# Kernel tuning notes

Measured on AMD Instinct MI355X. Metric: run time of the kernel, lower is better.

## Reference

```python
import jax, jax.numpy as jnp
import numpy as np

B, N, C = 4, 2048, 1024
H = 16
D = C // H  # 64
SCALE = D ** -0.5


def setup_inputs() -> dict:
    key = jax.random.key(0)
    ks = jax.random.split(key, 5)
    x = jax.random.normal(ks[0], (B, N, C), dtype=jnp.float32)
    qkv_w = jax.random.normal(ks[1], (3 * C, C), dtype=jnp.float32) * (C ** -0.5)
    qkv_b = jax.random.normal(ks[2], (3 * C,), dtype=jnp.float32) * 0.02
    bias_mask = jnp.zeros((3 * C,), dtype=jnp.float32)  # registered buffer, zeros
    proj_w = jax.random.normal(ks[3], (C, C), dtype=jnp.float32) * (C ** -0.5)
    proj_b = jax.random.normal(ks[4], (C,), dtype=jnp.float32) * 0.02
    return {"x": x, "qkv_w": qkv_w, "qkv_b": qkv_b, "bias_mask": bias_mask,
            "proj_w": proj_w, "proj_b": proj_b}


def reference(x, qkv_w, qkv_b, bias_mask, proj_w, proj_b):
    b, n, c = x.shape
    # qkv linear with masked bias (bias_mask is zeros -> effective zero bias)
    bias = qkv_b * bias_mask
    qkv = jnp.einsum('bnc,oc->bno', x, qkv_w) + bias  # [b, n, 3c]
    qkv = qkv.reshape(b, n, 3, H, D).transpose(2, 0, 3, 1, 4)  # [3, b, h, n, d]
    q, k, v = qkv[0], qkv[1], qkv[2]
    # explicit softmax attention (rope=None path)
    attn = jnp.einsum('bhqd,bhkd->bhqk', q, k) * SCALE  # [b, h, n, n]
    attn = jax.nn.softmax(attn, axis=-1)
    out = jnp.einsum('bhqk,bhkd->bhqd', attn, v)  # [b, h, n, d]
    out = out.transpose(0, 2, 1, 3).reshape(b, n, c)
    return jnp.einsum('bnc,oc->bno', out, proj_w) + proj_b
```

## Files before the change

kernel.cpp:

```cpp
#include <hip/hip_runtime.h>
#include <hip/hip_bf16.h>

#define B_ 4
#define N_ 2048
#define C_ 1024
#define H_ 16
#define D_ 64
#define QSCALE_ 0.1803368801f

typedef _Float16 f16;
typedef __attribute__((ext_vector_type(8))) _Float16 f16x8;
typedef __attribute__((ext_vector_type(4))) _Float16 f16x4;
typedef __attribute__((ext_vector_type(4))) float f32x4;
typedef __attribute__((ext_vector_type(16))) float f32x16;
typedef __attribute__((ext_vector_type(4))) int i32x4;
#define MFMA16(a, b, c) __builtin_amdgcn_mfma_f32_16x16x32_f16(a, b, c, 0, 0, 0)
#define MFMA32(a, b, c) __builtin_amdgcn_mfma_f32_32x32x16_f16(a, b, c, 0, 0, 0)

__device__ inline void gload_lds16(const f16* g, f16* l) {
    __builtin_amdgcn_global_load_lds(
        (const __attribute__((address_space(1))) void*)g,
        (__attribute__((address_space(3))) void*)l, 16, 0, 0);
}

__device__ inline int pkrtz(float a, float b) {
    return __builtin_bit_cast(int, __builtin_amdgcn_cvt_pkrtz(a, b));
}

#define NX_ 8388608u
#define NW1_ 3145728u
#define NW2_ 1048576u

__global__ __launch_bounds__(256) void convert_kernel(
    const float* __restrict__ x, const float* __restrict__ w1, const float* __restrict__ w2,
    f16* __restrict__ xo, f16* __restrict__ w1o, f16* __restrict__ w2o)
{
    const unsigned q = blockIdx.x * 256 + threadIdx.x;
    const unsigned i = q << 2;
    const float* src;
    f16* dst;
    if (i < NX_)              { src = x  + i;               dst = xo  + i; }
    else if (i < NX_ + NW1_)  { src = w1 + (i - NX_);       dst = w1o + (i - NX_); }
    else                      { src = w2 + (i - NX_ - NW1_); dst = w2o + (i - NX_ - NW1_); }
    const float4 v = *(const float4*)src;
    f16x4 h;
    h[0] = (f16)v.x; h[1] = (f16)v.y; h[2] = (f16)v.z; h[3] = (f16)v.w;
    *(f16x4*)dst = h;
}

__global__ __launch_bounds__(256) void qkv_gemm_f16(
    const f16* __restrict__ Xh,
    const f16* __restrict__ Wh,
    const float* __restrict__ qkv_b,
    const float* __restrict__ bias_mask,
    f16* __restrict__ Qh,
    f16* __restrict__ Kh,
    f16* __restrict__ Vt)
{
    __shared__ f16 As[128 * 64];
    __shared__ f16 Bs[128 * 64];
    const int tid  = threadIdx.x;
    const int bm   = blockIdx.x * 128;
    const int bo   = blockIdx.y * 128;
    const int lane = tid & 63, lo = lane & 15, grp = lane >> 4;
    const int wave = tid >> 6, wr = wave >> 1, wc = wave & 1;
    const int sr = tid >> 3, cg = tid & 7;
    const int scol = (cg ^ (sr & 7)) << 3;

    f32x4 acc[4][4];
    #pragma unroll
    for (int m = 0; m < 4; ++m)
        #pragma unroll
        for (int n = 0; n < 4; ++n) acc[m][n] = f32x4{0.f, 0.f, 0.f, 0.f};

    for (int k0 = 0; k0 < 1024; k0 += 64) {
        #pragma unroll
        for (int i = 0; i < 4; ++i) {
            const int tr = i * 32 + sr;
            gload_lds16(Xh + (size_t)(bm + tr) * 1024 + k0 + scol, As + (i * 2048 + tid * 8));
            gload_lds16(Wh + (size_t)(bo + tr) * 1024 + k0 + scol, Bs + (i * 2048 + tid * 8));
        }
        __syncthreads();
        #pragma unroll
        for (int kh = 0; kh < 2; ++kh) {
            f16x8 af[4], bfr[4];
            #pragma unroll
            for (int m = 0; m < 4; ++m) {
                const int row = wr * 64 + m * 16 + lo;
                af[m] = *(const f16x8*)(As + row * 64 + ((((kh << 2) + grp) << 3) ^ ((row & 7) << 3)));
            }
            #pragma unroll
            for (int n = 0; n < 4; ++n) {
                const int row = wc * 64 + n * 16 + lo;
                bfr[n] = *(const f16x8*)(Bs + row * 64 + ((((kh << 2) + grp) << 3) ^ ((row & 7) << 3)));
            }
            #pragma unroll
            for (int m = 0; m < 4; ++m)
                #pragma unroll
                for (int n = 0; n < 4; ++n)
                    acc[m][n] = MFMA16(af[m], bfr[n], acc[m][n]);
        }
        __syncthreads();
    }
    #pragma unroll
    for (int ni = 0; ni < 4; ++ni) {
        const int o = bo + wc * 64 + ni * 16 + lo;
        const float bias = qkv_b[o] * bias_mask[o];
        const int s = o >> 10, h = (o >> 6) & 15, d = o & 63;
        #pragma unroll
        for (int mi = 0; mi < 4; ++mi) {
            #pragma unroll
            for (int r = 0; r < 4; ++r) {
                const int m = bm + wr * 64 + mi * 16 + grp * 4 + r;
                const int b = m >> 11, n = m & (N_ - 1);
                const int bh = b * H_ + h;
                const float val = acc[mi][ni][r] + bias;
                if (s == 0)      Qh[((size_t)bh * N_ + n) * D_ + d] = (f16)(val * QSCALE_);
                else if (s == 1) Kh[((size_t)bh * N_ + n) * D_ + d] = (f16)val;
                else             Vt[((size_t)bh * D_ + d) * N_ + n] = (f16)val;
            }
        }
    }
}

__global__ __launch_bounds__(256) void proj_gemm_f16(
    const f16* __restrict__ Ah,
    const f16* __restrict__ Wh,
    const float* __restrict__ proj_b,
    float* __restrict__ Out)
{
    __shared__ f16 As[128 * 64];
    __shared__ f16 Bs[128 * 64];
    const int tid  = threadIdx.x;
    const int bm   = blockIdx.x * 128;
    const int bo   = blockIdx.y * 128;
    const int lane = tid & 63, lo = lane & 15, grp = lane >> 4;
    const int wave = tid >> 6, wr = wave >> 1, wc = wave & 1;
    const int sr = tid >> 3, cg = tid & 7;
    const int scol = (cg ^ (sr & 7)) << 3;

    f32x4 acc[4][4];
    #pragma unroll
    for (int m = 0; m < 4; ++m)
        #pragma unroll
        for (int n = 0; n < 4; ++n) acc[m][n] = f32x4{0.f, 0.f, 0.f, 0.f};

    for (int k0 = 0; k0 < 1024; k0 += 64) {
        #pragma unroll
        for (int i = 0; i < 4; ++i) {
            const int tr = i * 32 + sr;
            gload_lds16(Ah + (size_t)(bm + tr) * 1024 + k0 + scol, As + (i * 2048 + tid * 8));
            gload_lds16(Wh + (size_t)(bo + tr) * 1024 + k0 + scol, Bs + (i * 2048 + tid * 8));
        }
        __syncthreads();
        #pragma unroll
        for (int kh = 0; kh < 2; ++kh) {
            f16x8 af[4], bfr[4];
            #pragma unroll
            for (int m = 0; m < 4; ++m) {
                const int row = wr * 64 + m * 16 + lo;
                af[m] = *(const f16x8*)(As + row * 64 + ((((kh << 2) + grp) << 3) ^ ((row & 7) << 3)));
            }
            #pragma unroll
            for (int n = 0; n < 4; ++n) {
                const int row = wc * 64 + n * 16 + lo;
                bfr[n] = *(const f16x8*)(Bs + row * 64 + ((((kh << 2) + grp) << 3) ^ ((row & 7) << 3)));
            }
            #pragma unroll
            for (int m = 0; m < 4; ++m)
                #pragma unroll
                for (int n = 0; n < 4; ++n)
                    acc[m][n] = MFMA16(af[m], bfr[n], acc[m][n]);
        }
        __syncthreads();
    }
    #pragma unroll
    for (int ni = 0; ni < 4; ++ni) {
        const int o = bo + wc * 64 + ni * 16 + lo;
        const float pb = proj_b[o];
        #pragma unroll
        for (int mi = 0; mi < 4; ++mi) {
            #pragma unroll
            for (int r = 0; r < 4; ++r) {
                const int m = bm + wr * 64 + mi * 16 + grp * 4 + r;
                Out[(size_t)m * C_ + o] = acc[mi][ni][r] + pb;
            }
        }
    }
}

__global__ __launch_bounds__(256) void attn_fa15_kernel(
    const f16* __restrict__ Qb,
    const f16* __restrict__ Kb,
    const f16* __restrict__ Vt,
    f16* __restrict__ AO)
{
    __shared__ f16 Kt[2][128 * 64];
    __shared__ f16 Vb2[2][64 * 128];
    const int tid  = threadIdx.x;
    const int lane = tid & 63;
    const int lo   = lane & 31;
    const int hi   = lane >> 5;
    const int wave = tid >> 6;

    const int id   = blockIdx.x;
    const int xcd  = id & 7;
    const int j    = id >> 3;
    const int bh   = (xcd << 3) | (j >> 4);
    const int q0   = (j & 15) * 128 + wave * 32;
    const size_t base = (size_t)bh * (N_ * D_);

    const f16* Kp = Kb + base;
    const f16* Vp = Vt + base;

    f16x8 qf[4];
    #pragma unroll
    for (int dc = 0; dc < 4; ++dc)
        qf[dc] = *(const f16x8*)(Qb + base + (size_t)(q0 + lo) * D_ + dc * 16 + hi * 8);

#define STAGE_KV(BK, BV, KV0)                                                      \
    { _Pragma("unroll") for (int i_ = 0; i_ < 4; ++i_) {                           \
        const int si_ = i_ * 256 + tid;                                            \
        const int krow_ = si_ >> 3, kgrp_ = si_ & 7;                               \
        gload_lds16(Kp + (size_t)((KV0) + krow_) * D_ + ((kgrp_ ^ (krow_ & 7)) << 3), \
                    (BK) + si_ * 8);                                               \
        const int vrow_ = si_ >> 4, vslt_ = si_ & 15;                              \
        gload_lds16(Vp + (size_t)vrow_ * N_ + (KV0) + ((vslt_ ^ (vrow_ & 15)) << 3), \
                    (BV) + si_ * 8);                                               \
      } }

#define P_TO_FRAGS(P, PB1, PB2)                                                    \
    { int d0_ = pkrtz(P[0],  P[1]),  d1_ = pkrtz(P[2],  P[3]);                     \
      int d2_ = pkrtz(P[4],  P[5]),  d3_ = pkrtz(P[6],  P[7]);                     \
      int d4_ = pkrtz(P[8],  P[9]),  d5_ = pkrtz(P[10], P[11]);                    \
      int d6_ = pkrtz(P[12], P[13]), d7_ = pkrtz(P[14], P[15]);                    \
      const int x0_ = __shfl_xor(d0_, 32, 64), x1_ = __shfl_xor(d1_, 32, 64);      \
      const int x2_ = __shfl_xor(d2_, 32, 64), x3_ = __shfl_xor(d3_, 32, 64);      \
      const int x4_ = __shfl_xor(d4_, 32, 64), x5_ = __shfl_xor(d5_, 32, 64);      \
      const int x6_ = __shfl_xor(d6_, 32, 64), x7_ = __shfl_xor(d7_, 32, 64);      \
      i32x4 w1_, w2_;                                                              \
      w1_[0] = hi ? x2_ : d0_;  w1_[1] = hi ? x3_ : d1_;                           \
      w1_[2] = hi ? d2_ : x0_;  w1_[3] = hi ? d3_ : x1_;                           \
      w2_[0] = hi ? x6_ : d4_;  w2_[1] = hi ? x7_ : d5_;                           \
      w2_[2] = hi ? d6_ : x4_;  w2_[3] = hi ? d7_ : x5_;                           \
      PB1 = __builtin_bit_cast(f16x8, w1_);                                        \
      PB2 = __builtin_bit_cast(f16x8, w2_); }

    const f32x16 zero16 = {};
    f32x16 o0 = zero16, o1 = zero16;
    float lsum = 0.f;
    const int kx = (lo & 7) << 3;
    const int vx = lo & 15;

    STAGE_KV(Kt[0], Vb2[0], 0);
    int cur = 0;

    for (int t = 0; t < 16; ++t) {
        const int nxt = (t < 15) ? (t + 1) * 128 : 0;
        STAGE_KV(Kt[cur ^ 1], Vb2[cur ^ 1], nxt);
        asm volatile("s_waitcnt vmcnt(8)" ::: "memory");
        __builtin_amdgcn_s_barrier();
        __builtin_amdgcn_sched_barrier(0);

        const f16* kb = Kt[cur];
        const f16* vb = Vb2[cur];

        #pragma unroll
        for (int c = 0; c < 4; ++c) {
            f16x8 kf[4];
            #pragma unroll
            for (int dc = 0; dc < 4; ++dc)
                kf[dc] = *(const f16x8*)(kb + (c * 32 + lo) * 64 + ((((dc * 2 + hi) << 3)) ^ kx));
            __builtin_amdgcn_s_setprio(1);
            f32x16 s = MFMA32(kf[0], qf[0], zero16);
            s = MFMA32(kf[1], qf[1], s);
            s = MFMA32(kf[2], qf[2], s);
            s = MFMA32(kf[3], qf[3], s);
            __builtin_amdgcn_s_setprio(0);

            const f16x8 vf00 = *(const f16x8*)(vb + lo * 128 + (((c * 4 + hi) ^ vx) << 3));
            const f16x8 vf01 = *(const f16x8*)(vb + lo * 128 + (((c * 4 + 2 + hi) ^ vx) << 3));
            const f16x8 vf10 = *(const f16x8*)(vb + (32 + lo) * 128 + (((c * 4 + hi) ^ vx) << 3));
            const f16x8 vf11 = *(const f16x8*)(vb + (32 + lo) * 128 + (((c * 4 + 2 + hi) ^ vx) << 3));

            float p[16];
            #pragma unroll
            for (int r = 0; r < 16; ++r) p[r] = __builtin_amdgcn_exp2f(s[r]);
            lsum += (((p[0]+p[1])+(p[2]+p[3])) + ((p[4]+p[5])+(p[6]+p[7])))
                  + (((p[8]+p[9])+(p[10]+p[11])) + ((p[12]+p[13])+(p[14]+p[15])));
            f16x8 pb1, pb2;
            P_TO_FRAGS(p, pb1, pb2);

            __builtin_amdgcn_s_setprio(1);
            o0 = MFMA32(vf00, pb1, o0);
            o0 = MFMA32(vf01, pb2, o0);
            o1 = MFMA32(vf10, pb1, o1);
            o1 = MFMA32(vf11, pb2, o1);
            __builtin_amdgcn_s_setprio(0);
        }

        __builtin_amdgcn_sched_barrier(0);
        __builtin_amdgcn_s_barrier();
        cur ^= 1;
    }

    lsum += __shfl_xor(lsum, 32, 64);
    const int b = bh >> 4;
    const int h = bh & (H_ - 1);
    const float inv = 1.f / lsum;
    f16* outp = AO + ((size_t)(b * N_ + q0 + lo)) * C_ + h * D_;
    #pragma unroll
    for (int dh = 0; dh < 2; ++dh) {
        #pragma unroll
        for (int j2 = 0; j2 < 4; ++j2) {
            const int d0 = dh * 32 + 8 * j2 + 4 * hi;
            f16x4 st;
            #pragma unroll
            for (int e = 0; e < 4; ++e) {
                const float v = (dh == 0 ? o0[4 * j2 + e] : o1[4 * j2 + e]) * inv;
                st[e] = (f16)v;
            }
            *(f16x4*)(outp + d0) = st;
        }
    }
#undef STAGE_KV
#undef P_TO_FRAGS
}

extern "C" void kernel_launch(void* const* d_in, const int* in_sizes, int n_in,
                              void* d_out, int out_size, void* d_ws, size_t ws_size,
                              hipStream_t stream) {
    const float* x         = (const float*)d_in[0];
    const float* qkv_w     = (const float*)d_in[1];
    const float* qkv_b     = (const float*)d_in[2];
    const float* bias_mask = (const float*)d_in[3];
    const float* proj_w    = (const float*)d_in[4];
    const float* proj_b    = (const float*)d_in[5];
    float* out = (float*)d_out;

    const size_t NE = (size_t)B_ * H_ * N_ * D_;
    f16* Xh  = (f16*)d_ws;
    f16* Wh  = Xh + NE;
    f16* Ph  = Wh + NW1_;
    f16* Qh  = Ph + NW2_;
    f16* Kh  = Qh + NE;
    f16* Vt  = Kh + NE;
    f16* AOh = Vt + NE;

    dim3 blk(256);
    convert_kernel<<<12288, blk, 0, stream>>>(x, qkv_w, proj_w, Xh, Wh, Ph);
    qkv_gemm_f16<<<dim3(64, 24), blk, 0, stream>>>(Xh, Wh, qkv_b, bias_mask, Qh, Kh, Vt);
    attn_fa15_kernel<<<dim3(1024), blk, 0, stream>>>(Qh, Kh, Vt, AOh);
    proj_gemm_f16<<<dim3(64, 8), blk, 0, stream>>>(AOh, Ph, proj_b, out);
}
```

Before: 225.2 us.

## Rewrite QKV GEMM with 256x256 tiles, 8 waves and double-buffered LDS prefetch

```diff
diff --git a/kernel.cpp b/kernel.cpp
--- a/kernel.cpp
+++ b/kernel.cpp
@@ -48,7 +48,7 @@
     *(f16x4*)dst = h;
 }
 
-__global__ __launch_bounds__(256) void qkv_gemm_f16(
+__global__ __launch_bounds__(512) void qkv_gemm_8p(
     const f16* __restrict__ Xh,
     const f16* __restrict__ Wh,
     const float* __restrict__ qkv_b,
@@ -57,70 +57,105 @@
     f16* __restrict__ Kh,
     f16* __restrict__ Vt)
 {
-    __shared__ f16 As[128 * 64];
-    __shared__ f16 Bs[128 * 64];
+    __shared__ f16 As[2][256 * 64];
+    __shared__ f16 Bs[2][256 * 64];
     const int tid  = threadIdx.x;
-    const int bm   = blockIdx.x * 128;
-    const int bo   = blockIdx.y * 128;
     const int lane = tid & 63, lo = lane & 15, grp = lane >> 4;
-    const int wave = tid >> 6, wr = wave >> 1, wc = wave & 1;
-    const int sr = tid >> 3, cg = tid & 7;
-    const int scol = (cg ^ (sr & 7)) << 3;
-
-    f32x4 acc[4][4];
-    #pragma unroll
-    for (int m = 0; m < 4; ++m)
+    const int wave = tid >> 6;
+    const int wr   = wave >> 2, wc = wave & 3;
+    const int bm   = blockIdx.x * 256;
+    const int bo   = blockIdx.y * 256;
+
+    f32x4 acc[8][4];
+    #pragma unroll
+    for (int m = 0; m < 8; ++m)
         #pragma unroll
         for (int n = 0; n < 4; ++n) acc[m][n] = f32x4{0.f, 0.f, 0.f, 0.f};
 
-    for (int k0 = 0; k0 < 1024; k0 += 64) {
-        #pragma unroll
-        for (int i = 0; i < 4; ++i) {
-            const int tr = i * 32 + sr;
-            gload_lds16(Xh + (size_t)(bm + tr) * 1024 + k0 + scol, As + (i * 2048 + tid * 8));
-            gload_lds16(Wh + (size_t)(bo + tr) * 1024 + k0 + scol, Bs + (i * 2048 + tid * 8));
-        }
-        __syncthreads();
-        #pragma unroll
-        for (int kh = 0; kh < 2; ++kh) {
-            f16x8 af[4], bfr[4];
-            #pragma unroll
-            for (int m = 0; m < 4; ++m) {
-                const int row = wr * 64 + m * 16 + lo;
-                af[m] = *(const f16x8*)(As + row * 64 + ((((kh << 2) + grp) << 3) ^ ((row & 7) << 3)));
-            }
-            #pragma unroll
-            for (int n = 0; n < 4; ++n) {
+#define STAGE_T(BA, BB, K0)                                                     \
+    { _Pragma("unroll") for (int i_ = 0; i_ < 4; ++i_) {                        \
+        const int si_ = i_ * 512 + tid;                                         \
+        const int row_ = si_ >> 3, g_ = si_ & 7;                                \
+        const int sc_ = (g_ ^ (row_ & 7)) << 3;                                 \
+        gload_lds16(Xh + (size_t)(bm + row_) * 1024 + (K0) + sc_, (BA) + si_ * 8); \
+        gload_lds16(Wh + (size_t)(bo + row_) * 1024 + (K0) + sc_, (BB) + si_ * 8); \
+      } }
+
+    STAGE_T(As[0], Bs[0], 0);
+    asm volatile("s_waitcnt vmcnt(0)" ::: "memory");
+    __syncthreads();
+    int cur = 0;
+
+    for (int t = 0; t < 16; ++t) {
+        const int k0n = (t < 15) ? (t + 1) * 64 : 0;
+        __builtin_amdgcn_s_barrier();
+        STAGE_T(As[cur ^ 1], Bs[cur ^ 1], k0n);
+        asm volatile("s_waitcnt vmcnt(8)" ::: "memory");
+        __builtin_amdgcn_s_barrier();
+        __builtin_amdgcn_sched_barrier(0);
+
+        const f16* ab = As[cur];
+        const f16* bb = Bs[cur];
+
+        f16x8 bf[4][2];
+        #pragma unroll
+        for (int n = 0; n < 4; ++n)
+            #pragma unroll
+            for (int kh = 0; kh < 2; ++kh) {
                 const int row = wc * 64 + n * 16 + lo;
-                bfr[n] = *(const f16x8*)(Bs + row * 64 + ((((kh << 2) + grp) << 3) ^ ((row & 7) << 3)));
-            }
-            #pragma unroll
-            for (int m = 0; m < 4; ++m)
+                bf[n][kh] = *(const f16x8*)(bb + row * 64 +
+                              ((((kh << 2) + grp) << 3) ^ ((row & 7) << 3)));
+            }
+
+        #pragma unroll
+        for (int ph = 0; ph < 4; ++ph) {
+            if (ph) {
+                __builtin_amdgcn_sched_barrier(0);
+                __builtin_amdgcn_s_barrier();
+            }
+            f16x8 af[2][2];
+            #pragma unroll
+            for (int mi = 0; mi < 2; ++mi)
+                #pragma unroll
+                for (int kh = 0; kh < 2; ++kh) {
+                    const int row = wr * 128 + (ph * 2 + mi) * 16 + lo;
+                    af[mi][kh] = *(const f16x8*)(ab + row * 64 +
+                                  ((((kh << 2) + grp) << 3) ^ ((row & 7) << 3)));
+                }
+            __builtin_amdgcn_s_setprio(1);
+            #pragma unroll
+            for (int mi = 0; mi < 2; ++mi)
                 #pragma unroll
                 for (int n = 0; n < 4; ++n)
-                    acc[m][n] = MFMA16(af[m], bfr[n], acc[m][n]);
-        }
-        __syncthreads();
-    }
-    #pragma unroll
-    for (int ni = 0; ni < 4; ++ni) {
-        const int o = bo + wc * 64 + ni * 16 + lo;
+                    #pragma unroll
+                    for (int kh = 0; kh < 2; ++kh)
+                        acc[ph * 2 + mi][n] = MFMA16(af[mi][kh], bf[n][kh], acc[ph * 2 + mi][n]);
+            __builtin_amdgcn_s_setprio(0);
+        }
+        __builtin_amdgcn_sched_barrier(0);
+        cur ^= 1;
+    }
+
+    #pragma unroll
+    for (int nf = 0; nf < 4; ++nf) {
+        const int o = bo + wc * 64 + nf * 16 + lo;
         const float bias = qkv_b[o] * bias_mask[o];
         const int s = o >> 10, h = (o >> 6) & 15, d = o & 63;
         #pragma unroll
-        for (int mi = 0; mi < 4; ++mi) {
+        for (int mf = 0; mf < 8; ++mf) {
             #pragma unroll
             for (int r = 0; r < 4; ++r) {
-                const int m = bm + wr * 64 + mi * 16 + grp * 4 + r;
+                const int m = bm + wr * 128 + mf * 16 + grp * 4 + r;
                 const int b = m >> 11, n = m & (N_ - 1);
                 const int bh = b * H_ + h;
-                const float val = acc[mi][ni][r] + bias;
+                const float val = acc[mf][nf][r] + bias;
                 if (s == 0)      Qh[((size_t)bh * N_ + n) * D_ + d] = (f16)(val * QSCALE_);
                 else if (s == 1) Kh[((size_t)bh * N_ + n) * D_ + d] = (f16)val;
                 else             Vt[((size_t)bh * D_ + d) * N_ + n] = (f16)val;
             }
         }
     }
+#undef STAGE_T
 }
 
 __global__ __launch_bounds__(256) void proj_gemm_f16(
@@ -349,7 +384,7 @@
 
     dim3 blk(256);
     convert_kernel<<<12288, blk, 0, stream>>>(x, qkv_w, proj_w, Xh, Wh, Ph);
-    qkv_gemm_f16<<<dim3(64, 24), blk, 0, stream>>>(Xh, Wh, qkv_b, bias_mask, Qh, Kh, Vt);
+    qkv_gemm_8p<<<dim3(32, 12), dim3(512), 0, stream>>>(Xh, Wh, qkv_b, bias_mask, Qh, Kh, Vt);
     attn_fa15_kernel<<<dim3(1024), blk, 0, stream>>>(Qh, Kh, Vt, AOh);
     proj_gemm_f16<<<dim3(64, 8), blk, 0, stream>>>(AOh, Ph, proj_b, out);
 }
```

New measurement: 245.5 us. +9.0%, slower.
